# Performance work log

Hardware: AMD Instinct MI355X
Metric: run time of the kernel (lower is better)

The kernel has to match this reference:

```python
import math
import jax, jax.numpy as jnp
import numpy as np

B, S, D = 8, 920, 1536
H, HD = 4, 384            # num heads, head dim; all_head = H*HD = 1536
MAX_POS = 920
L = 2 * MAX_POS - 1       # 1839 relative positions


def setup_inputs() -> dict:
    key = jax.random.key(0)
    k1, k2, k3, k4, k5 = jax.random.split(key, 5)
    return {
        "hidden_states": jax.random.normal(k1, (B, S, D), dtype=jnp.float32),
        "w_query": jax.random.normal(k2, (D, H * HD), dtype=jnp.float32) * 0.02,
        "w_key": jax.random.normal(k3, (D, H * HD), dtype=jnp.float32) * 0.02,
        "w_value": jax.random.normal(k4, (D, H * HD), dtype=jnp.float32) * 0.02,
        "distance_embedding": jax.random.normal(k5, (L, HD), dtype=jnp.float32) * 0.02,
    }


def reshape_fortran(x, shape):
    # Matches torch reference: reverse-permute, C reshape of reversed shape, reverse-permute back.
    x = jnp.transpose(x, tuple(reversed(range(x.ndim))))
    x = jnp.reshape(x, tuple(reversed(shape)))
    return jnp.transpose(x, tuple(reversed(range(len(shape)))))


def relative_position_embedding_rotate(scores):
    # scores: [B, H, L, S]
    scores = jnp.transpose(scores, (0, 2, 3, 1))  # [B, L, S, H]
    b, hs, s, h = scores.shape
    scores = jnp.concatenate([scores, jnp.zeros((b, s, s, h), scores.dtype)], axis=1)
    scores = reshape_fortran(scores, [b, (hs + s) * s, 1, h])
    scores = scores[:, : (s + hs - 1) * s]
    scores = reshape_fortran(scores, [b, hs + s - 1, s, h])
    halfpoint = hs // 2
    scores = scores[:, halfpoint : halfpoint + s]          # [B, S, S, H]
    scores = jnp.transpose(scores, (0, 2, 1, 3))           # transpose(1,2)
    return jnp.transpose(scores, (0, 3, 1, 2))             # [B, H, S, S]


def reference(hidden_states, w_query, w_key, w_value, distance_embedding):
    inv = 1.0 / math.sqrt(HD)
    q = (hidden_states @ w_query) * inv                    # [B, S, H*HD]
    k = hidden_states @ w_key
    v = hidden_states @ w_value

    def heads(x):  # [B,S,H*HD] -> [B,H,S,HD]
        return jnp.transpose(x.reshape(B, S, H, HD), (0, 2, 1, 3))

    q, k, v = heads(q), heads(k), heads(v)

    scores = jnp.einsum("bhqd,bhkd->bhqk", q, k)           # [B,H,S,S]
    rel = jnp.einsum("ld,bhsd->bhls", distance_embedding, q)  # [B,H,L,S]
    scores = scores + relative_position_embedding_rotate(rel)

    probs = jax.nn.softmax(scores, axis=-1)
    ctx = jnp.einsum("bhqk,bhkd->bhqd", probs, v)          # [B,H,S,HD]
    ctx = jnp.transpose(ctx, (0, 2, 1, 3)).reshape(B, S, H * HD)
    return ctx
```

## Files before the change

kernel.cpp:

```cpp
#include <hip/hip_runtime.h>

#define S_LEN 920
#define DMODEL 1536
#define NH 4
#define HD 384
#define LREL 1839
#define BATCH 8
#define MTOT (BATCH * S_LEN)
#define KPAD 960
#define NBH (BATCH * NH)

#define CHS   5652480UL
#define BSLAB 2826240UL
#define KOFF  1413120UL

#define EB_BYTES 1412352UL
#define VT_BYTES 23592960UL

typedef __attribute__((ext_vector_type(8))) short  s16x8;
typedef __attribute__((ext_vector_type(4))) short  s16x4;
typedef __attribute__((ext_vector_type(8))) __bf16 bf16x8;
typedef __attribute__((ext_vector_type(4))) float  f32x4;

__device__ __forceinline__ short f2b(float x) {
  unsigned u = __builtin_bit_cast(unsigned, x);
  unsigned r = (u + 0x7FFFu + ((u >> 16) & 1u)) >> 16;
  return (short)r;
}
__device__ __forceinline__ float b2f(short s) {
  unsigned u = ((unsigned)(unsigned short)s) << 16;
  return __builtin_bit_cast(float, u);
}

__device__ __forceinline__ void load_lds16(const short* g, short* lds) {
  __builtin_amdgcn_global_load_lds(
      (const __attribute__((address_space(1))) void*)g,
      (__attribute__((address_space(3))) void*)lds, 16, 0, 0);
}

__device__ __forceinline__ f32x4 mfma_bf16(s16x8 a, s16x8 b, f32x4 c) {
  return __builtin_amdgcn_mfma_f32_16x16x32_bf16(
      __builtin_bit_cast(bf16x8, a), __builtin_bit_cast(bf16x8, b), c, 0, 0, 0);
}

__device__ __forceinline__ s16x8 frag_swz(const short* base, int row, int kk, int lq) {
  int byte = (row << 7) + (kk << 6) + (lq << 4);
  byte ^= (row & 7) << 4;
  return *(const s16x8*)((const char*)base + byte);
}

template <int NT>
__device__ __forceinline__ void gemm_pipe(short* smem,
    const short* __restrict__ A, int ldA, int mClamp, int m0,
    const short* __restrict__ B, int ldB, int nClamp, int n0,
    f32x4 acc[4][6]) {
  short* const A0 = smem;
  short* const B0 = smem + 16384;
  short* const A1 = smem + 28672;
  short* const B1 = smem + 45056;

  const int tid = threadIdx.x, w = tid >> 6, lane = tid & 63;
  const int lr = lane & 15, lq = lane >> 4;
  const int wr = w >> 1, wc = w & 1;

  const short* pa[4]; int la[4];
  const short* pb[3]; int lb[3];
  {
    const int rl = lane >> 3, c = lane & 7;
#pragma unroll
    for (int i = 0; i < 4; ++i) {
      int r = w * 32 + i * 8 + rl;
      int ra = m0 + r; if (ra > mClamp) ra = mClamp;
      pa[i] = A + (size_t)ra * ldA + ((c ^ (r & 7)) * 8);
      la[i] = (w * 32 + i * 8) * 64;
    }
#pragma unroll
    for (int i = 0; i < 3; ++i) {
      int r = w * 24 + i * 8 + rl;
      int rb = n0 + r; if (rb > nClamp) rb = nClamp;
      pb[i] = B + (size_t)rb * ldB + ((c ^ (r & 7)) * 8);
      lb[i] = (w * 24 + i * 8) * 64;
    }
  }

#pragma unroll
  for (int i = 0; i < 4; ++i)
#pragma unroll
    for (int j = 0; j < 6; ++j) acc[i][j] = (f32x4){0.f, 0.f, 0.f, 0.f};

#pragma unroll
  for (int i = 0; i < 4; ++i) load_lds16(pa[i], A0 + la[i]);
#pragma unroll
  for (int i = 0; i < 3; ++i) load_lds16(pb[i], B0 + lb[i]);

  for (int kt = 0; kt < NT; ++kt) {
    short* const Ab = (kt & 1) ? A1 : A0;
    short* const Bb = (kt & 1) ? B1 : B0;
    short* const An = (kt & 1) ? A0 : A1;
    short* const Bn = (kt & 1) ? B0 : B1;

    if (kt + 1 < NT) {
      const int k0 = (kt + 1) * 64;
#pragma unroll
      for (int i = 0; i < 4; ++i) load_lds16(pa[i] + k0, An + la[i]);
#pragma unroll
      for (int i = 0; i < 3; ++i) load_lds16(pb[i] + k0, Bn + lb[i]);
      asm volatile("s_waitcnt vmcnt(7)" ::: "memory");
    } else {
      asm volatile("s_waitcnt vmcnt(0)" ::: "memory");
    }
    __builtin_amdgcn_sched_barrier(0);
    __builtin_amdgcn_s_barrier();
    __builtin_amdgcn_sched_barrier(0);

    s16x8 a[4], bb[3];
#pragma unroll
    for (int f = 0; f < 4; ++f) a[f] = frag_swz(Ab, wr * 64 + f * 16 + lr, 0, lq);
#pragma unroll
    for (int f = 0; f < 3; ++f) bb[f] = frag_swz(Bb, wc * 96 + f * 16 + lr, 0, lq);
    __builtin_amdgcn_s_barrier();
    __builtin_amdgcn_s_setprio(1);
#pragma unroll
    for (int i = 0; i < 4; ++i)
#pragma unroll
      for (int j = 0; j < 3; ++j) acc[i][j] = mfma_bf16(a[i], bb[j], acc[i][j]);
    __builtin_amdgcn_s_setprio(0);
    __builtin_amdgcn_s_barrier();
#pragma unroll
    for (int f = 0; f < 3; ++f) bb[f] = frag_swz(Bb, wc * 96 + (3 + f) * 16 + lr, 0, lq);
    __builtin_amdgcn_s_barrier();
    __builtin_amdgcn_s_setprio(1);
#pragma unroll
    for (int i = 0; i < 4; ++i)
#pragma unroll
      for (int j = 0; j < 3; ++j) acc[i][3 + j] = mfma_bf16(a[i], bb[j], acc[i][3 + j]);
    __builtin_amdgcn_s_setprio(0);
    __builtin_amdgcn_s_barrier();
#pragma unroll
    for (int f = 0; f < 4; ++f) a[f] = frag_swz(Ab, wr * 64 + f * 16 + lr, 1, lq);
#pragma unroll
    for (int f = 0; f < 3; ++f) bb[f] = frag_swz(Bb, wc * 96 + f * 16 + lr, 1, lq);
    __builtin_amdgcn_s_barrier();
    __builtin_amdgcn_s_setprio(1);
#pragma unroll
    for (int i = 0; i < 4; ++i)
#pragma unroll
      for (int j = 0; j < 3; ++j) acc[i][j] = mfma_bf16(a[i], bb[j], acc[i][j]);
    __builtin_amdgcn_s_setprio(0);
    __builtin_amdgcn_s_barrier();
#pragma unroll
    for (int f = 0; f < 3; ++f) bb[f] = frag_swz(Bb, wc * 96 + (3 + f) * 16 + lr, 1, lq);
    __builtin_amdgcn_s_barrier();
    __builtin_amdgcn_s_setprio(1);
#pragma unroll
    for (int i = 0; i < 4; ++i)
#pragma unroll
      for (int j = 0; j < 3; ++j) acc[i][3 + j] = mfma_bf16(a[i], bb[j], acc[i][3 + j]);
    __builtin_amdgcn_s_setprio(0);
    __builtin_amdgcn_s_barrier();
  }
}

__global__ void k_cast(const float* __restrict__ X, short* __restrict__ O, int n4) {
  int i = blockIdx.x * blockDim.x + threadIdx.x;
  if (i >= n4) return;
  float4 v = ((const float4*)X)[i];
  s16x4 o = {f2b(v.x), f2b(v.y), f2b(v.z), f2b(v.w)};
  *(s16x4*)&O[(size_t)i * 4] = o;
}

__global__ void k_transpose_w(const float* __restrict__ W0, const float* __restrict__ W1,
                              const float* __restrict__ W2, short* __restrict__ Wt) {
  const float* W = (blockIdx.z == 0) ? W0 : ((blockIdx.z == 1) ? W1 : W2);
  short* O = Wt + (size_t)blockIdx.z * DMODEL * DMODEL;
  __shared__ float t[32][33];
  int tx = threadIdx.x, ty = threadIdx.y;
  int n0 = blockIdx.x * 32, k0 = blockIdx.y * 32;
#pragma unroll
  for (int i = 0; i < 4; ++i)
    t[ty + i * 8][tx] = W[(size_t)(k0 + ty + i * 8) * DMODEL + n0 + tx];
  __syncthreads();
#pragma unroll
  for (int i = 0; i < 4; ++i)
    O[(size_t)(n0 + ty + i * 8) * DMODEL + k0 + tx] = f2b(t[tx][ty + i * 8]);
}

__global__ void k_zero_vtpad(short* __restrict__ Vt) {
  int idx = blockIdx.x * blockDim.x + threadIdx.x;
  if (idx >= NBH * HD * (KPAD - S_LEN)) return;
  int bhd = idx / (KPAD - S_LEN);
  int s = S_LEN + idx - bhd * (KPAD - S_LEN);
  Vt[(size_t)bhd * KPAD + s] = 0;
}

#define QKV_NT (DMODEL / 64)

__global__ __launch_bounds__(512, 2) void k_gemm_qkv(const short* __restrict__ Xb,
                                                     const short* __restrict__ Wt,
                                                     short* __restrict__ out16,
                                                     short* __restrict__ Vt) {
  __shared__ short smem[57344];
  const int z = blockIdx.z;
  const int t = blockIdx.x;
  const int t2 = (t & 7) * 29 + (t >> 3);
  const int m0 = (t2 >> 3) * 256;
  const int n0 = (t2 & 7) * 192;

  const int tid = threadIdx.x, w = tid >> 6, lane = tid & 63;
  const int lr = lane & 15, lq = lane >> 4;
  const int wr = w >> 1, wc = w & 1;

  f32x4 acc[4][6];
  gemm_pipe<QKV_NT>(smem, Xb, DMODEL, MTOT - 1, m0,
                    Wt + (size_t)z * DMODEL * DMODEL, DMODEL, DMODEL - 1, n0, acc);

  __syncthreads();
  const float inv = 0.05103103630798287f;
  if (z != 2) {
    short* T = smem;
#pragma unroll
    for (int i = 0; i < 4; ++i)
#pragma unroll
      for (int j = 0; j < 6; ++j) {
        int ml = wr * 64 + i * 16 + lq * 4;
        int nl = wc * 96 + j * 16 + lr;
#pragma unroll
        for (int r = 0; r < 4; ++r) {
          float v = acc[i][j][r];
          T[(ml + r) * 200 + nl] = f2b(z == 0 ? v * inv : v);
        }
      }
    __syncthreads();
    for (int u = 0; u < 12; ++u) {
      int unit = u * 512 + tid;
      int ml = unit / 24, c = unit - ml * 24;
      int m = m0 + ml;
      if (m < MTOT) {
        int b = m / S_LEN, s = m - b * S_LEN;
        short* dst = out16 + (size_t)(b >> 1) * CHS + (size_t)(b & 1) * BSLAB +
                     (z == 1 ? KOFF : 0UL) + (size_t)s * DMODEL + n0 + c * 8;
        *(s16x8*)dst = *(const s16x8*)&T[ml * 200 + c * 8];
      }
    }
  } else {
    short* T = smem;
#pragma unroll
    for (int i = 0; i < 4; ++i)
#pragma unroll
      for (int j = 0; j < 6; ++j) {
        int ml = wr * 64 + i * 16 + lq * 4;
        int nl = wc * 96 + j * 16 + lr;
#pragma unroll
        for (int r = 0; r < 4; ++r)
          T[nl * 264 + ml + r] = f2b(acc[i][j][r]);
      }
    __syncthreads();
    const int h = n0 / HD;
    const int d0 = n0 - h * HD;
    for (int u = 0; u < 12; ++u) {
      int unit = u * 512 + tid;
      int nl = unit >> 5, c = unit & 31;
      int m = m0 + c * 8;
      if (m < MTOT) {
        int b = m / S_LEN, s = m - b * S_LEN;
        size_t row = (size_t)(b * NH + h) * HD + d0 + nl;
        *(s16x8*)&Vt[row * KPAD + s] = *(const s16x8*)&T[nl * 264 + c * 8];
      }
    }
  }
}

#define FKV 192
#define FNT 5

#define WAITVM(N) { asm volatile("s_waitcnt vmcnt(" #N ")" ::: "memory"); \
  __builtin_amdgcn_sched_barrier(0); __builtin_amdgcn_s_barrier(); \
  __builtin_amdgcn_sched_barrier(0); }

#define LBAR { asm volatile("s_waitcnt lgkmcnt(0)" ::: "memory"); \
  __builtin_amdgcn_sched_barrier(0); __builtin_amdgcn_s_barrier(); \
  __builtin_amdgcn_sched_barrier(0); }

#define NOISSUE { }

#define STAGE_E(BUF_, C, L0) { \
  _Pragma("unroll") for (int i_ = 0; i_ < 4; ++i_) { \
    int r_ = w * 32 + i_ * 8 + rl; \
    int rg_ = (L0) + r_; rg_ = rg_ < 0 ? 0 : (rg_ > LREL - 1 ? LREL - 1 : rg_); \
    load_lds16(Eb + (size_t)rg_ * HD + ((cs ^ (r_ & 7)) * 8) + (C) * 64, \
               (BUF_) + (w * 32 + i_ * 8) * 64); } }

#define STAGE_K(BUF_, C) { \
  _Pragma("unroll") for (int i_ = 0; i_ < 3; ++i_) { \
    int r_ = w * 24 + i_ * 8 + rl; \
    int rg_ = kv0 + r_; if (rg_ > S_LEN - 1) rg_ = S_LEN - 1; \
    load_lds16(Kp + (size_t)rg_ * DMODEL + ((cs ^ (r_ & 7)) * 8) + (C) * 64, \
               (BUF_) + (w * 24 + i_ * 8) * 64); } }

#define STAGE_V(BUF_, HF, SC) { \
  _Pragma("unroll") for (int i_ = 0; i_ < 3; ++i_) { \
    int r_ = w * 24 + i_ * 8 + rl; \
    load_lds16(Vb + (size_t)((HF) * 192 + r_) * KPAD + kv0 + (SC) * 64 + ((cs ^ (r_ & 7)) * 8), \
               (BUF_) + (w * 24 + i_ * 8) * 64); } }

#define SLOT_T(C, BUFR, ISSUE, WVM) { ISSUE; WVM; \
  s16x8 a_[2], b_[2][4]; \
  _Pragma("unroll") for (int k_ = 0; k_ < 2; ++k_) { \
    a_[k_] = frag_swz(QL + (C) * 2048, wm * 16 + lr, k_, lq); \
    _Pragma("unroll") for (int j_ = 0; j_ < 4; ++j_) \
      b_[k_][j_] = frag_swz((BUFR), wn * 64 + j_ * 16 + lr, k_, lq); } \
  __builtin_amdgcn_s_setprio(1); \
  _Pragma("unroll") for (int k_ = 0; k_ < 2; ++k_) \
    _Pragma("unroll") for (int j_ = 0; j_ < 4; ++j_) \
      acc_t[j_] = mfma_bf16(a_[k_], b_[k_][j_], acc_t[j_]); \
  __builtin_amdgcn_s_setprio(0); __builtin_amdgcn_s_barrier(); }

#define SLOT_S(C, BUFR, ISSUE, WVM) { ISSUE; WVM; \
  s16x8 a_[2], b_[2][3]; \
  _Pragma("unroll") for (int k_ = 0; k_ < 2; ++k_) { \
    a_[k_] = frag_swz(QL + (C) * 2048, wm * 16 + lr, k_, lq); \
    _Pragma("unroll") for (int j_ = 0; j_ < 3; ++j_) \
      b_[k_][j_] = frag_swz((BUFR), wn * 48 + j_ * 16 + lr, k_, lq); } \
  __builtin_amdgcn_s_setprio(1); \
  _Pragma("unroll") for (int k_ = 0; k_ < 2; ++k_) \
    _Pragma("unroll") for (int j_ = 0; j_ < 3; ++j_) \
      acc_s[j_] = mfma_bf16(a_[k_], b_[k_][j_], acc_s[j_]); \
  __builtin_amdgcn_s_setprio(0); __builtin_amdgcn_s_barrier(); }

#define SLOT_PV(SC, HF, BUFR, ISSUE, WVM) { ISSUE; WVM; \
  s16x8 a_[2], b_[2][3]; \
  _Pragma("unroll") for (int k_ = 0; k_ < 2; ++k_) { \
    a_[k_] = frag_swz(TLP + (SC) * 2048, wm * 16 + lr, k_, lq); \
    _Pragma("unroll") for (int j_ = 0; j_ < 3; ++j_) \
      b_[k_][j_] = frag_swz((BUFR), wn * 48 + j_ * 16 + lr, k_, lq); } \
  __builtin_amdgcn_s_setprio(1); \
  _Pragma("unroll") for (int k_ = 0; k_ < 2; ++k_) \
    _Pragma("unroll") for (int j_ = 0; j_ < 3; ++j_) \
      acc_o[(HF) * 3 + j_] = mfma_bf16(a_[k_], b_[k_][j_], acc_o[(HF) * 3 + j_]); \
  __builtin_amdgcn_s_setprio(0); __builtin_amdgcn_s_barrier(); }

__global__ __launch_bounds__(512, 1) void k_fused(const short* __restrict__ out16,
                                                  const short* __restrict__ Vt,
                                                  const short* __restrict__ Eb,
                                                  float* __restrict__ O, int half) {
  __shared__ short smem[70144];
  short* const QL  = smem;
  short* const B0h = smem + 12288;
  short* const B1h = smem + 28672;
  short* const B2h = smem + 45056;
  short* const TLP = smem + 61440;
  float* const pmax = (float*)(smem + 69632);
  float* const psum = pmax + 128;

  const int f  = blockIdx.x;
  const int f2 = (f & 7) * 58 + (f >> 3);
  const int mt = f2 % 29, bhl = f2 / 29;
  const int bh = half * 16 + bhl, b = bh >> 2, h = bh & 3;
  const int m0 = mt * 32;

  const int tid = threadIdx.x, w = tid >> 6, lane = tid & 63;
  const int lr = lane & 15, lq = lane >> 4;
  const int wm = w >> 2, wn = w & 3;
  const int rl = lane >> 3, cs = lane & 7;

  const short* Qp = out16 + (size_t)(b >> 1) * CHS + (size_t)(b & 1) * BSLAB + h * HD;
  const short* Kp = Qp + KOFF;
  const short* Vb = Vt + (size_t)bh * HD * KPAD;
  float* Ob = O + (size_t)bhl * S_LEN * HD;

  f32x4 acc_o[6];
  float Mst[4], Lst[4];
#pragma unroll
  for (int j = 0; j < 6; ++j) acc_o[j] = (f32x4){0.f, 0.f, 0.f, 0.f};
#pragma unroll
  for (int r = 0; r < 4; ++r) { Mst[r] = -1e30f; Lst[r] = 0.f; }

#pragma unroll
  for (int k = 0; k < 3; ++k) {
    int idx = k * 8 + w;
    int chunk = idx >> 2;
    int row = (idx & 3) * 8 + rl;
    int rg = m0 + row; if (rg > S_LEN - 1) rg = S_LEN - 1;
    load_lds16(Qp + (size_t)rg * DMODEL + chunk * 64 + ((cs ^ (row & 7)) * 8),
               QL + idx * 512);
  }
  { const int l00 = 888 - m0; STAGE_E(B0h, 0, l00); STAGE_E(B1h, 1, l00); }

  for (int t = 0; t < FNT; ++t) {
    const int kv0 = t * FKV;
    const int l0 = kv0 - m0 + 888;

    f32x4 acc_t[4];
#pragma unroll
    for (int j = 0; j < 4; ++j) acc_t[j] = (f32x4){0.f, 0.f, 0.f, 0.f};

    SLOT_T(0, B0h, STAGE_E(B2h, 2, l0), WAITVM(8));
    SLOT_T(1, B1h, STAGE_E(B0h, 3, l0), WAITVM(8));
    SLOT_T(2, B2h, STAGE_E(B1h, 4, l0), WAITVM(8));
    SLOT_T(3, B0h, STAGE_E(B2h, 5, l0), WAITVM(8));
    SLOT_T(4, B1h, STAGE_K(B0h, 0),     WAITVM(7));
    SLOT_T(5, B2h, STAGE_K(B1h, 1),     WAITVM(6));

#pragma unroll
    for (int j = 0; j < 4; ++j)
#pragma unroll
      for (int r = 0; r < 4; ++r) {
        int row = wm * 16 + lq * 4 + r;
        int col = wn * 64 + j * 16 + lr;
        TLP[row * 256 + col] = f2b(acc_t[j][r]);
      }
    LBAR;

    f32x4 acc_s[3];
#pragma unroll
    for (int j = 0; j < 3; ++j) acc_s[j] = (f32x4){0.f, 0.f, 0.f, 0.f};

    SLOT_S(0, B0h, STAGE_K(B2h, 2),    WAITVM(6));
    SLOT_S(1, B1h, STAGE_K(B0h, 3),    WAITVM(6));
    SLOT_S(2, B2h, STAGE_K(B1h, 4),    WAITVM(6));
    SLOT_S(3, B0h, STAGE_K(B2h, 5),    WAITVM(6));
    SLOT_S(4, B1h, STAGE_V(B0h, 0, 0), WAITVM(6));
    SLOT_S(5, B2h, STAGE_V(B1h, 0, 1), WAITVM(6));

#pragma unroll
    for (int j = 0; j < 3; ++j) {
      int jpl = wn * 48 + j * 16 + lr;
      int jp = kv0 + jpl;
#pragma unroll
      for (int r = 0; r < 4; ++r) {
        int row = wm * 16 + lq * 4 + r;
        float x = acc_s[j][r] + b2f(TLP[row * 256 + (jpl - row + 31)]);
        acc_s[j][r] = (jp < S_LEN) ? x : -1e30f;
      }
    }
    {
      float tm[4];
#pragma unroll
      for (int r = 0; r < 4; ++r) {
        float v = fmaxf(fmaxf(acc_s[0][r], acc_s[1][r]), acc_s[2][r]);
#pragma unroll
        for (int o = 1; o < 16; o <<= 1) v = fmaxf(v, __shfl_xor(v, o));
        tm[r] = v;
      }
      if (lr == 0) {
#pragma unroll
        for (int r = 0; r < 4; ++r)
          pmax[wn * 32 + wm * 16 + lq * 4 + r] = tm[r];
      }
    }
    LBAR;
    float fexp[4], ps[4];
#pragma unroll
    for (int r = 0; r < 4; ++r) {
      int row = wm * 16 + lq * 4 + r;
      float M2 = fmaxf(fmaxf(pmax[row], pmax[32 + row]),
                       fmaxf(pmax[64 + row], pmax[96 + row]));
      M2 = fmaxf(M2, Mst[r]);
      fexp[r] = __expf(Mst[r] - M2);
      Mst[r] = M2;
    }
#pragma unroll
    for (int r = 0; r < 4; ++r) {
      float s0 = 0.f;
#pragma unroll
      for (int j = 0; j < 3; ++j) {
        float p = __expf(acc_s[j][r] - Mst[r]);
        acc_s[j][r] = p;
        s0 += p;
      }
#pragma unroll
      for (int o = 1; o < 16; o <<= 1) s0 += __shfl_xor(s0, o);
      ps[r] = s0;
#pragma unroll
      for (int jj = 0; jj < 6; ++jj) acc_o[jj][r] *= fexp[r];
    }
    if (lr == 0) {
#pragma unroll
      for (int r = 0; r < 4; ++r)
        psum[wn * 32 + wm * 16 + lq * 4 + r] = ps[r];
    }
    LBAR;
#pragma unroll
    for (int r = 0; r < 4; ++r) {
      int row = wm * 16 + lq * 4 + r;
      float ts = psum[row] + psum[32 + row] + psum[64 + row] + psum[96 + row];
      Lst[r] = Lst[r] * fexp[r] + ts;
    }
#pragma unroll
    for (int j = 0; j < 3; ++j) {
      int c192 = wn * 48 + j * 16 + lr;
      int sc = c192 >> 6, c64 = c192 & 63;
#pragma unroll
      for (int r = 0; r < 4; ++r) {
        int row = wm * 16 + lq * 4 + r;
        int byte = sc * 4096 + row * 128 + ((c64 * 2) ^ ((row & 7) * 16));
        *(short*)((char*)TLP + byte) = f2b(acc_s[j][r]);
      }
    }
    LBAR;

    SLOT_PV(0, 0, B0h, STAGE_V(B2h, 0, 2), WAITVM(6));
    SLOT_PV(1, 0, B1h, STAGE_V(B0h, 1, 0), WAITVM(6));
    SLOT_PV(2, 0, B2h, STAGE_V(B1h, 1, 1), WAITVM(6));
    SLOT_PV(0, 1, B0h, STAGE_V(B2h, 1, 2), WAITVM(6));
    if (t < FNT - 1) {
      SLOT_PV(1, 1, B1h, STAGE_E(B0h, 0, l0 + FKV), WAITVM(7));
      SLOT_PV(2, 1, B2h, STAGE_E(B1h, 1, l0 + FKV), WAITVM(8));
    } else {
      SLOT_PV(1, 1, B1h, NOISSUE, WAITVM(3));
      SLOT_PV(2, 1, B2h, NOISSUE, WAITVM(0));
    }
  }

#pragma unroll
  for (int r = 0; r < 4; ++r) {
    int m = m0 + wm * 16 + lq * 4 + r;
    if (m < S_LEN) {
      float rs = 1.0f / Lst[r];
#pragma unroll
      for (int jj = 0; jj < 6; ++jj) {
        int d = (jj / 3) * 192 + wn * 48 + (jj % 3) * 16 + lr;
        Ob[(size_t)m * HD + d] = acc_o[jj][r] * rs;
      }
    }
  }
}

__global__ __launch_bounds__(256) void k_copy_o(const float* __restrict__ O,
                                                float* __restrict__ out, int b0) {
  int i = blockIdx.x * 256 + threadIdx.x;
  if (i >= 16 * S_LEN * HD / 4) return;
  const int per_bh = S_LEN * HD / 4;
  int bhl = i / per_bh, rem = i - bhl * per_bh;
  int m = rem / (HD / 4), d4 = rem - m * (HD / 4);
  int b = b0 + (bhl >> 2), h = bhl & 3;
  float4 v = ((const float4*)O)[i];
  ((float4*)out)[((size_t)(b * S_LEN + m) * DMODEL + h * HD + d4 * 4) >> 2] = v;
}

extern "C" void kernel_launch(void* const* d_in, const int* in_sizes, int n_in,
                              void* d_out, int out_size, void* d_ws, size_t ws_size,
                              hipStream_t stream) {
  const float* hs = (const float*)d_in[0];
  const float* wq = (const float*)d_in[1];
  const float* wk = (const float*)d_in[2];
  const float* wv = (const float*)d_in[3];
  const float* de = (const float*)d_in[4];
  char* ws = (char*)d_ws;

  short* Xb = (short*)(ws + 0);
  short* Wt = (short*)(ws + 22609920UL);
  short* Eb = (short*)(ws + 36765696UL);
  short* Vt = (short*)(ws + 36765696UL + EB_BYTES);
  float* Og = (float*)(ws + 0);
  short* out16 = (short*)d_out;

  k_cast<<<(MTOT * DMODEL / 4 + 255) / 256, 256, 0, stream>>>(hs, Xb, MTOT * DMODEL / 4);
  k_cast<<<(LREL * HD / 4 + 255) / 256, 256, 0, stream>>>(de, Eb, LREL * HD / 4);
  k_transpose_w<<<dim3(48, 48, 3), dim3(32, 8, 1), 0, stream>>>(wq, wk, wv, Wt);
  k_zero_vtpad<<<(NBH * HD * (KPAD - S_LEN) + 255) / 256, 256, 0, stream>>>(Vt);

  k_gemm_qkv<<<dim3(232, 1, 3), 512, 0, stream>>>(Xb, Wt, out16, Vt);

  for (int hf = 0; hf < 2; ++hf) {
    k_fused<<<dim3(464), 512, 0, stream>>>(out16, Vt, Eb, Og, hf);
    k_copy_o<<<dim3(5520), 256, 0, stream>>>(Og, (float*)d_out, hf * 4);
  }
}
```

Before: 435.8 us.

## Retile QKV GEMM to 192x192 with triple-buffered LDS prefetch

Replaces the 256x192 double-buffered QKV GEMM with a 192x192 tile using a three-stage LDS ring, so global loads run two k-steps ahead. The warp layout changes to 2x4 with 96x48 per warp, and the grid grows from 232 to 312 blocks per z to fill more CUs. LDS use rises to 144KB and launch bounds drop to one block per CU, which trades occupancy for deeper prefetch. The epilogue strides are adjusted to the new tile shape.

```diff
diff --git a/kernel.cpp b/kernel.cpp
--- a/kernel.cpp
+++ b/kernel.cpp
@@ -49,118 +49,6 @@
   return *(const s16x8*)((const char*)base + byte);
 }
 
-template <int NT>
-__device__ __forceinline__ void gemm_pipe(short* smem,
-    const short* __restrict__ A, int ldA, int mClamp, int m0,
-    const short* __restrict__ B, int ldB, int nClamp, int n0,
-    f32x4 acc[4][6]) {
-  short* const A0 = smem;
-  short* const B0 = smem + 16384;
-  short* const A1 = smem + 28672;
-  short* const B1 = smem + 45056;
-
-  const int tid = threadIdx.x, w = tid >> 6, lane = tid & 63;
-  const int lr = lane & 15, lq = lane >> 4;
-  const int wr = w >> 1, wc = w & 1;
-
-  const short* pa[4]; int la[4];
-  const short* pb[3]; int lb[3];
-  {
-    const int rl = lane >> 3, c = lane & 7;
-#pragma unroll
-    for (int i = 0; i < 4; ++i) {
-      int r = w * 32 + i * 8 + rl;
-      int ra = m0 + r; if (ra > mClamp) ra = mClamp;
-      pa[i] = A + (size_t)ra * ldA + ((c ^ (r & 7)) * 8);
-      la[i] = (w * 32 + i * 8) * 64;
-    }
-#pragma unroll
-    for (int i = 0; i < 3; ++i) {
-      int r = w * 24 + i * 8 + rl;
-      int rb = n0 + r; if (rb > nClamp) rb = nClamp;
-      pb[i] = B + (size_t)rb * ldB + ((c ^ (r & 7)) * 8);
-      lb[i] = (w * 24 + i * 8) * 64;
-    }
-  }
-
-#pragma unroll
-  for (int i = 0; i < 4; ++i)
-#pragma unroll
-    for (int j = 0; j < 6; ++j) acc[i][j] = (f32x4){0.f, 0.f, 0.f, 0.f};
-
-#pragma unroll
-  for (int i = 0; i < 4; ++i) load_lds16(pa[i], A0 + la[i]);
-#pragma unroll
-  for (int i = 0; i < 3; ++i) load_lds16(pb[i], B0 + lb[i]);
-
-  for (int kt = 0; kt < NT; ++kt) {
-    short* const Ab = (kt & 1) ? A1 : A0;
-    short* const Bb = (kt & 1) ? B1 : B0;
-    short* const An = (kt & 1) ? A0 : A1;
-    short* const Bn = (kt & 1) ? B0 : B1;
-
-    if (kt + 1 < NT) {
-      const int k0 = (kt + 1) * 64;
-#pragma unroll
-      for (int i = 0; i < 4; ++i) load_lds16(pa[i] + k0, An + la[i]);
-#pragma unroll
-      for (int i = 0; i < 3; ++i) load_lds16(pb[i] + k0, Bn + lb[i]);
-      asm volatile("s_waitcnt vmcnt(7)" ::: "memory");
-    } else {
-      asm volatile("s_waitcnt vmcnt(0)" ::: "memory");
-    }
-    __builtin_amdgcn_sched_barrier(0);
-    __builtin_amdgcn_s_barrier();
-    __builtin_amdgcn_sched_barrier(0);
-
-    s16x8 a[4], bb[3];
-#pragma unroll
-    for (int f = 0; f < 4; ++f) a[f] = frag_swz(Ab, wr * 64 + f * 16 + lr, 0, lq);
-#pragma unroll
-    for (int f = 0; f < 3; ++f) bb[f] = frag_swz(Bb, wc * 96 + f * 16 + lr, 0, lq);
-    __builtin_amdgcn_s_barrier();
-    __builtin_amdgcn_s_setprio(1);
-#pragma unroll
-    for (int i = 0; i < 4; ++i)
-#pragma unroll
-      for (int j = 0; j < 3; ++j) acc[i][j] = mfma_bf16(a[i], bb[j], acc[i][j]);
-    __builtin_amdgcn_s_setprio(0);
-    __builtin_amdgcn_s_barrier();
-#pragma unroll
-    for (int f = 0; f < 3; ++f) bb[f] = frag_swz(Bb, wc * 96 + (3 + f) * 16 + lr, 0, lq);
-    __builtin_amdgcn_s_barrier();
-    __builtin_amdgcn_s_setprio(1);
-#pragma unroll
-    for (int i = 0; i < 4; ++i)
-#pragma unroll
-      for (int j = 0; j < 3; ++j) acc[i][3 + j] = mfma_bf16(a[i], bb[j], acc[i][3 + j]);
-    __builtin_amdgcn_s_setprio(0);
-    __builtin_amdgcn_s_barrier();
-#pragma unroll
-    for (int f = 0; f < 4; ++f) a[f] = frag_swz(Ab, wr * 64 + f * 16 + lr, 1, lq);
-#pragma unroll
-    for (int f = 0; f < 3; ++f) bb[f] = frag_swz(Bb, wc * 96 + f * 16 + lr, 1, lq);
-    __builtin_amdgcn_s_barrier();
-    __builtin_amdgcn_s_setprio(1);
-#pragma unroll
-    for (int i = 0; i < 4; ++i)
-#pragma unroll
-      for (int j = 0; j < 3; ++j) acc[i][j] = mfma_bf16(a[i], bb[j], acc[i][j]);
-    __builtin_amdgcn_s_setprio(0);
-    __builtin_amdgcn_s_barrier();
-#pragma unroll
-    for (int f = 0; f < 3; ++f) bb[f] = frag_swz(Bb, wc * 96 + (3 + f) * 16 + lr, 1, lq);
-    __builtin_amdgcn_s_barrier();
-    __builtin_amdgcn_s_setprio(1);
-#pragma unroll
-    for (int i = 0; i < 4; ++i)
-#pragma unroll
-      for (int j = 0; j < 3; ++j) acc[i][3 + j] = mfma_bf16(a[i], bb[j], acc[i][3 + j]);
-    __builtin_amdgcn_s_setprio(0);
-    __builtin_amdgcn_s_barrier();
-  }
-}
-
 __global__ void k_cast(const float* __restrict__ X, short* __restrict__ O, int n4) {
   int i = blockIdx.x * blockDim.x + threadIdx.x;
   if (i >= n4) return;
@@ -194,36 +82,112 @@
 }
 
 #define QKV_NT (DMODEL / 64)
-
-__global__ __launch_bounds__(512, 2) void k_gemm_qkv(const short* __restrict__ Xb,
+#define QBUF   24576
+
+__global__ __launch_bounds__(512, 1) void k_gemm_qkv(const short* __restrict__ Xb,
                                                      const short* __restrict__ Wt,
                                                      short* __restrict__ out16,
                                                      short* __restrict__ Vt) {
-  __shared__ short smem[57344];
+  __shared__ short smem[73728];
   const int z = blockIdx.z;
   const int t = blockIdx.x;
-  const int t2 = (t & 7) * 29 + (t >> 3);
-  const int m0 = (t2 >> 3) * 256;
-  const int n0 = (t2 & 7) * 192;
+  const int t2 = (t & 7) * 39 + (t >> 3);
+  const int m_idx = t2 >> 3;
+  const int n_idx = t2 & 7;
+  const int m0 = m_idx * 192;
+  const int n0 = n_idx * 192;
 
   const int tid = threadIdx.x, w = tid >> 6, lane = tid & 63;
   const int lr = lane & 15, lq = lane >> 4;
-  const int wr = w >> 1, wc = w & 1;
-
-  f32x4 acc[4][6];
-  gemm_pipe<QKV_NT>(smem, Xb, DMODEL, MTOT - 1, m0,
-                    Wt + (size_t)z * DMODEL * DMODEL, DMODEL, DMODEL - 1, n0, acc);
+  const int wm = w >> 2, wn = w & 3;
+
+  const short* const Bg = Wt + (size_t)z * DMODEL * DMODEL;
+
+  const short* pa[3]; const short* pb[3]; int lofs[3];
+  {
+    const int rl = lane >> 3, c = lane & 7;
+#pragma unroll
+    for (int i = 0; i < 3; ++i) {
+      int r = w * 24 + i * 8 + rl;
+      int ra = m0 + r; if (ra > MTOT - 1) ra = MTOT - 1;
+      pa[i] = Xb + (size_t)ra * DMODEL + ((c ^ (r & 7)) * 8);
+      pb[i] = Bg + (size_t)(n0 + r) * DMODEL + ((c ^ (r & 7)) * 8);
+      lofs[i] = (w * 24 + i * 8) * 64;
+    }
+  }
+
+  f32x4 acc[6][3];
+#pragma unroll
+  for (int i = 0; i < 6; ++i)
+#pragma unroll
+    for (int j = 0; j < 3; ++j) acc[i][j] = (f32x4){0.f, 0.f, 0.f, 0.f};
+
+  short* P0 = smem;
+  short* P1 = smem + QBUF;
+  short* P2 = smem + 2 * QBUF;
+
+#pragma unroll
+  for (int i = 0; i < 3; ++i) {
+    load_lds16(pa[i], P0 + lofs[i]);
+    load_lds16(pb[i], P0 + 12288 + lofs[i]);
+  }
+#pragma unroll
+  for (int i = 0; i < 3; ++i) {
+    load_lds16(pa[i] + 64, P1 + lofs[i]);
+    load_lds16(pb[i] + 64, P1 + 12288 + lofs[i]);
+  }
+
+  for (int kt = 0; kt < QKV_NT; ++kt) {
+    short* const Ab = P0;
+    short* const Bb = P0 + 12288;
+
+    if (kt + 2 < QKV_NT) {
+      const int k0 = (kt + 2) * 64;
+#pragma unroll
+      for (int i = 0; i < 3; ++i) {
+        load_lds16(pa[i] + k0, P2 + lofs[i]);
+        load_lds16(pb[i] + k0, P2 + 12288 + lofs[i]);
+      }
+      asm volatile("s_waitcnt vmcnt(12)" ::: "memory");
+    } else if (kt + 1 < QKV_NT) {
+      asm volatile("s_waitcnt vmcnt(6)" ::: "memory");
+    } else {
+      asm volatile("s_waitcnt vmcnt(0)" ::: "memory");
+    }
+    __builtin_amdgcn_sched_barrier(0);
+    __builtin_amdgcn_s_barrier();
+    __builtin_amdgcn_sched_barrier(0);
+
+#pragma unroll
+    for (int kk = 0; kk < 2; ++kk) {
+      s16x8 a[6], bb[3];
+#pragma unroll
+      for (int f = 0; f < 6; ++f) a[f] = frag_swz(Ab, wm * 96 + f * 16 + lr, kk, lq);
+#pragma unroll
+      for (int f = 0; f < 3; ++f) bb[f] = frag_swz(Bb, wn * 48 + f * 16 + lr, kk, lq);
+      __builtin_amdgcn_s_barrier();
+      __builtin_amdgcn_s_setprio(1);
+#pragma unroll
+      for (int i = 0; i < 6; ++i)
+#pragma unroll
+        for (int j = 0; j < 3; ++j) acc[i][j] = mfma_bf16(a[i], bb[j], acc[i][j]);
+      __builtin_amdgcn_s_setprio(0);
+      __builtin_amdgcn_s_barrier();
+    }
+
+    short* tmp = P0; P0 = P1; P1 = P2; P2 = tmp;
+  }
 
   __syncthreads();
   const float inv = 0.05103103630798287f;
   if (z != 2) {
     short* T = smem;
 #pragma unroll
-    for (int i = 0; i < 4; ++i)
-#pragma unroll
-      for (int j = 0; j < 6; ++j) {
-        int ml = wr * 64 + i * 16 + lq * 4;
-        int nl = wc * 96 + j * 16 + lr;
+    for (int i = 0; i < 6; ++i)
+#pragma unroll
+      for (int j = 0; j < 3; ++j) {
+        int ml = wm * 96 + i * 16 + lq * 4;
+        int nl = wn * 48 + j * 16 + lr;
 #pragma unroll
         for (int r = 0; r < 4; ++r) {
           float v = acc[i][j][r];
@@ -231,7 +195,8 @@
         }
       }
     __syncthreads();
-    for (int u = 0; u < 12; ++u) {
+#pragma unroll
+    for (int u = 0; u < 9; ++u) {
       int unit = u * 512 + tid;
       int ml = unit / 24, c = unit - ml * 24;
       int m = m0 + ml;
@@ -245,26 +210,27 @@
   } else {
     short* T = smem;
 #pragma unroll
-    for (int i = 0; i < 4; ++i)
-#pragma unroll
-      for (int j = 0; j < 6; ++j) {
-        int ml = wr * 64 + i * 16 + lq * 4;
-        int nl = wc * 96 + j * 16 + lr;
+    for (int i = 0; i < 6; ++i)
+#pragma unroll
+      for (int j = 0; j < 3; ++j) {
+        int ml = wm * 96 + i * 16 + lq * 4;
+        int nl = wn * 48 + j * 16 + lr;
 #pragma unroll
         for (int r = 0; r < 4; ++r)
-          T[nl * 264 + ml + r] = f2b(acc[i][j][r]);
+          T[nl * 200 + ml + r] = f2b(acc[i][j][r]);
       }
     __syncthreads();
     const int h = n0 / HD;
     const int d0 = n0 - h * HD;
-    for (int u = 0; u < 12; ++u) {
+#pragma unroll
+    for (int u = 0; u < 9; ++u) {
       int unit = u * 512 + tid;
-      int nl = unit >> 5, c = unit & 31;
+      int nl = unit / 24, c = unit - nl * 24;
       int m = m0 + c * 8;
       if (m < MTOT) {
         int b = m / S_LEN, s = m - b * S_LEN;
         size_t row = (size_t)(b * NH + h) * HD + d0 + nl;
-        *(s16x8*)&Vt[row * KPAD + s] = *(const s16x8*)&T[nl * 264 + c * 8];
+        *(s16x8*)&Vt[row * KPAD + s] = *(const s16x8*)&T[nl * 200 + c * 8];
       }
     }
   }
@@ -560,7 +526,7 @@
   k_transpose_w<<<dim3(48, 48, 3), dim3(32, 8, 1), 0, stream>>>(wq, wk, wv, Wt);
   k_zero_vtpad<<<(NBH * HD * (KPAD - S_LEN) + 255) / 256, 256, 0, stream>>>(Vt);
 
-  k_gemm_qkv<<<dim3(232, 1, 3), 512, 0, stream>>>(Xb, Wt, out16, Vt);
+  k_gemm_qkv<<<dim3(312, 1, 3), 512, 0, stream>>>(Xb, Wt, out16, Vt);
 
   for (int hf = 0; hf < 2; ++hf) {
     k_fused<<<dim3(464), 512, 0, stream>>>(out16, Vt, Eb, Og, hf);
```

After: 446.4 us. +2.4%, slower.

## Load E/K/V MFMA operands directly from global memory instead of LDS staging

Applied to the files above, without the earlier changes.

Drops the triple-buffered LDS staging pipeline for the E, K and V tiles. Each wave now reads its MFMA B-fragments straight from global memory through per-lane pointers. LDS use falls from about 140KB to about 42KB, and launch bounds move from 1 to 4 blocks per CU so several blocks can share a CU. The cost is no data sharing across waves: the 2 wm-row waves each reload the same fragments. It also loses the explicit prefetch overlap, so performance now depends on cache hit rates and on occupancy hiding the global memory latency.

```diff
diff --git a/kernel.cpp b/kernel.cpp
--- a/kernel.cpp
+++ b/kernel.cpp
@@ -273,83 +273,18 @@
 #define FKV 192
 #define FNT 5
 
-#define WAITVM(N) { asm volatile("s_waitcnt vmcnt(" #N ")" ::: "memory"); \
-  __builtin_amdgcn_sched_barrier(0); __builtin_amdgcn_s_barrier(); \
-  __builtin_amdgcn_sched_barrier(0); }
-
 #define LBAR { asm volatile("s_waitcnt lgkmcnt(0)" ::: "memory"); \
   __builtin_amdgcn_sched_barrier(0); __builtin_amdgcn_s_barrier(); \
   __builtin_amdgcn_sched_barrier(0); }
 
-#define NOISSUE { }
-
-#define STAGE_E(BUF_, C, L0) { \
-  _Pragma("unroll") for (int i_ = 0; i_ < 4; ++i_) { \
-    int r_ = w * 32 + i_ * 8 + rl; \
-    int rg_ = (L0) + r_; rg_ = rg_ < 0 ? 0 : (rg_ > LREL - 1 ? LREL - 1 : rg_); \
-    load_lds16(Eb + (size_t)rg_ * HD + ((cs ^ (r_ & 7)) * 8) + (C) * 64, \
-               (BUF_) + (w * 32 + i_ * 8) * 64); } }
-
-#define STAGE_K(BUF_, C) { \
-  _Pragma("unroll") for (int i_ = 0; i_ < 3; ++i_) { \
-    int r_ = w * 24 + i_ * 8 + rl; \
-    int rg_ = kv0 + r_; if (rg_ > S_LEN - 1) rg_ = S_LEN - 1; \
-    load_lds16(Kp + (size_t)rg_ * DMODEL + ((cs ^ (r_ & 7)) * 8) + (C) * 64, \
-               (BUF_) + (w * 24 + i_ * 8) * 64); } }
-
-#define STAGE_V(BUF_, HF, SC) { \
-  _Pragma("unroll") for (int i_ = 0; i_ < 3; ++i_) { \
-    int r_ = w * 24 + i_ * 8 + rl; \
-    load_lds16(Vb + (size_t)((HF) * 192 + r_) * KPAD + kv0 + (SC) * 64 + ((cs ^ (r_ & 7)) * 8), \
-               (BUF_) + (w * 24 + i_ * 8) * 64); } }
-
-#define SLOT_T(C, BUFR, ISSUE, WVM) { ISSUE; WVM; \
-  s16x8 a_[2], b_[2][4]; \
-  _Pragma("unroll") for (int k_ = 0; k_ < 2; ++k_) { \
-    a_[k_] = frag_swz(QL + (C) * 2048, wm * 16 + lr, k_, lq); \
-    _Pragma("unroll") for (int j_ = 0; j_ < 4; ++j_) \
-      b_[k_][j_] = frag_swz((BUFR), wn * 64 + j_ * 16 + lr, k_, lq); } \
-  __builtin_amdgcn_s_setprio(1); \
-  _Pragma("unroll") for (int k_ = 0; k_ < 2; ++k_) \
-    _Pragma("unroll") for (int j_ = 0; j_ < 4; ++j_) \
-      acc_t[j_] = mfma_bf16(a_[k_], b_[k_][j_], acc_t[j_]); \
-  __builtin_amdgcn_s_setprio(0); __builtin_amdgcn_s_barrier(); }
-
-#define SLOT_S(C, BUFR, ISSUE, WVM) { ISSUE; WVM; \
-  s16x8 a_[2], b_[2][3]; \
-  _Pragma("unroll") for (int k_ = 0; k_ < 2; ++k_) { \
-    a_[k_] = frag_swz(QL + (C) * 2048, wm * 16 + lr, k_, lq); \
-    _Pragma("unroll") for (int j_ = 0; j_ < 3; ++j_) \
-      b_[k_][j_] = frag_swz((BUFR), wn * 48 + j_ * 16 + lr, k_, lq); } \
-  __builtin_amdgcn_s_setprio(1); \
-  _Pragma("unroll") for (int k_ = 0; k_ < 2; ++k_) \
-    _Pragma("unroll") for (int j_ = 0; j_ < 3; ++j_) \
-      acc_s[j_] = mfma_bf16(a_[k_], b_[k_][j_], acc_s[j_]); \
-  __builtin_amdgcn_s_setprio(0); __builtin_amdgcn_s_barrier(); }
-
-#define SLOT_PV(SC, HF, BUFR, ISSUE, WVM) { ISSUE; WVM; \
-  s16x8 a_[2], b_[2][3]; \
-  _Pragma("unroll") for (int k_ = 0; k_ < 2; ++k_) { \
-    a_[k_] = frag_swz(TLP + (SC) * 2048, wm * 16 + lr, k_, lq); \
-    _Pragma("unroll") for (int j_ = 0; j_ < 3; ++j_) \
-      b_[k_][j_] = frag_swz((BUFR), wn * 48 + j_ * 16 + lr, k_, lq); } \
-  __builtin_amdgcn_s_setprio(1); \
-  _Pragma("unroll") for (int k_ = 0; k_ < 2; ++k_) \
-    _Pragma("unroll") for (int j_ = 0; j_ < 3; ++j_) \
-      acc_o[(HF) * 3 + j_] = mfma_bf16(a_[k_], b_[k_][j_], acc_o[(HF) * 3 + j_]); \
-  __builtin_amdgcn_s_setprio(0); __builtin_amdgcn_s_barrier(); }
-
-__global__ __launch_bounds__(512, 1) void k_fused(const short* __restrict__ out16,
+__global__ __launch_bounds__(512, 4) void k_fused(const short* __restrict__ out16,
                                                   const short* __restrict__ Vt,
                                                   const short* __restrict__ Eb,
                                                   float* __restrict__ O, int half) {
-  __shared__ short smem[70144];
+  __shared__ short smem[20992];
   short* const QL  = smem;
-  short* const B0h = smem + 12288;
-  short* const B1h = smem + 28672;
-  short* const B2h = smem + 45056;
-  short* const TLP = smem + 61440;
-  float* const pmax = (float*)(smem + 69632);
+  short* const TLP = smem + 12288;
+  float* const pmax = (float*)(smem + 20480);
   float* const psum = pmax + 128;
 
   const int f  = blockIdx.x;
@@ -384,22 +319,45 @@
     load_lds16(Qp + (size_t)rg * DMODEL + chunk * 64 + ((cs ^ (row & 7)) * 8),
                QL + idx * 512);
   }
-  { const int l00 = 888 - m0; STAGE_E(B0h, 0, l00); STAGE_E(B1h, 1, l00); }
+  asm volatile("s_waitcnt vmcnt(0)" ::: "memory");
+  __builtin_amdgcn_s_barrier();
+
+  const short* vp[2][3];
+#pragma unroll
+  for (int hf = 0; hf < 2; ++hf)
+#pragma unroll
+    for (int j = 0; j < 3; ++j)
+      vp[hf][j] = Vb + (size_t)(hf * 192 + wn * 48 + j * 16 + lr) * KPAD + lq * 8;
 
   for (int t = 0; t < FNT; ++t) {
     const int kv0 = t * FKV;
     const int l0 = kv0 - m0 + 888;
 
+    const short* ep[4];
+#pragma unroll
+    for (int j = 0; j < 4; ++j) {
+      int l = l0 + wn * 64 + j * 16 + lr;
+      l = l < 0 ? 0 : (l > LREL - 1 ? LREL - 1 : l);
+      ep[j] = Eb + (size_t)l * HD + lq * 8;
+    }
     f32x4 acc_t[4];
 #pragma unroll
     for (int j = 0; j < 4; ++j) acc_t[j] = (f32x4){0.f, 0.f, 0.f, 0.f};
-
-    SLOT_T(0, B0h, STAGE_E(B2h, 2, l0), WAITVM(8));
-    SLOT_T(1, B1h, STAGE_E(B0h, 3, l0), WAITVM(8));
-    SLOT_T(2, B2h, STAGE_E(B1h, 4, l0), WAITVM(8));
-    SLOT_T(3, B0h, STAGE_E(B2h, 5, l0), WAITVM(8));
-    SLOT_T(4, B1h, STAGE_K(B0h, 0),     WAITVM(7));
-    SLOT_T(5, B2h, STAGE_K(B1h, 1),     WAITVM(6));
+#pragma unroll
+    for (int c = 0; c < 6; ++c) {
+      s16x8 bt[2][4];
+#pragma unroll
+      for (int kk = 0; kk < 2; ++kk)
+#pragma unroll
+        for (int j = 0; j < 4; ++j)
+          bt[kk][j] = *(const s16x8*)(ep[j] + c * 64 + kk * 32);
+      s16x8 a0 = frag_swz(QL + c * 2048, wm * 16 + lr, 0, lq);
+      s16x8 a1 = frag_swz(QL + c * 2048, wm * 16 + lr, 1, lq);
+#pragma unroll
+      for (int j = 0; j < 4; ++j) acc_t[j] = mfma_bf16(a0, bt[0][j], acc_t[j]);
+#pragma unroll
+      for (int j = 0; j < 4; ++j) acc_t[j] = mfma_bf16(a1, bt[1][j], acc_t[j]);
+    }
 
 #pragma unroll
     for (int j = 0; j < 4; ++j)
@@ -411,16 +369,31 @@
       }
     LBAR;
 
+    const short* kp[3];
+#pragma unroll
+    for (int j = 0; j < 3; ++j) {
+      int rg = kv0 + wn * 48 + j * 16 + lr;
+      if (rg > S_LEN - 1) rg = S_LEN - 1;
+      kp[j] = Kp + (size_t)rg * DMODEL + lq * 8;
+    }
     f32x4 acc_s[3];
 #pragma unroll
     for (int j = 0; j < 3; ++j) acc_s[j] = (f32x4){0.f, 0.f, 0.f, 0.f};
-
-    SLOT_S(0, B0h, STAGE_K(B2h, 2),    WAITVM(6));
-    SLOT_S(1, B1h, STAGE_K(B0h, 3),    WAITVM(6));
-    SLOT_S(2, B2h, STAGE_K(B1h, 4),    WAITVM(6));
-    SLOT_S(3, B0h, STAGE_K(B2h, 5),    WAITVM(6));
-    SLOT_S(4, B1h, STAGE_V(B0h, 0, 0), WAITVM(6));
-    SLOT_S(5, B2h, STAGE_V(B1h, 0, 1), WAITVM(6));
+#pragma unroll
+    for (int c = 0; c < 6; ++c) {
+      s16x8 bk[2][3];
+#pragma unroll
+      for (int kk = 0; kk < 2; ++kk)
+#pragma unroll
+        for (int j = 0; j < 3; ++j)
+          bk[kk][j] = *(const s16x8*)(kp[j] + c * 64 + kk * 32);
+      s16x8 a0 = frag_swz(QL + c * 2048, wm * 16 + lr, 0, lq);
+      s16x8 a1 = frag_swz(QL + c * 2048, wm * 16 + lr, 1, lq);
+#pragma unroll
+      for (int j = 0; j < 3; ++j) acc_s[j] = mfma_bf16(a0, bk[0][j], acc_s[j]);
+#pragma unroll
+      for (int j = 0; j < 3; ++j) acc_s[j] = mfma_bf16(a1, bk[1][j], acc_s[j]);
+    }
 
 #pragma unroll
     for (int j = 0; j < 3; ++j) {
@@ -499,17 +472,26 @@
     }
     LBAR;
 
-    SLOT_PV(0, 0, B0h, STAGE_V(B2h, 0, 2), WAITVM(6));
-    SLOT_PV(1, 0, B1h, STAGE_V(B0h, 1, 0), WAITVM(6));
-    SLOT_PV(2, 0, B2h, STAGE_V(B1h, 1, 1), WAITVM(6));
-    SLOT_PV(0, 1, B0h, STAGE_V(B2h, 1, 2), WAITVM(6));
-    if (t < FNT - 1) {
-      SLOT_PV(1, 1, B1h, STAGE_E(B0h, 0, l0 + FKV), WAITVM(7));
-      SLOT_PV(2, 1, B2h, STAGE_E(B1h, 1, l0 + FKV), WAITVM(8));
-    } else {
-      SLOT_PV(1, 1, B1h, NOISSUE, WAITVM(3));
-      SLOT_PV(2, 1, B2h, NOISSUE, WAITVM(0));
-    }
+#pragma unroll
+    for (int hf = 0; hf < 2; ++hf)
+#pragma unroll
+      for (int sc = 0; sc < 3; ++sc) {
+        s16x8 bv[2][3];
+#pragma unroll
+        for (int kk = 0; kk < 2; ++kk)
+#pragma unroll
+          for (int j = 0; j < 3; ++j)
+            bv[kk][j] = *(const s16x8*)(vp[hf][j] + kv0 + sc * 64 + kk * 32);
+        s16x8 a0 = frag_swz(TLP + sc * 2048, wm * 16 + lr, 0, lq);
+        s16x8 a1 = frag_swz(TLP + sc * 2048, wm * 16 + lr, 1, lq);
+#pragma unroll
+        for (int j = 0; j < 3; ++j)
+          acc_o[hf * 3 + j] = mfma_bf16(a0, bv[0][j], acc_o[hf * 3 + j]);
+#pragma unroll
+        for (int j = 0; j < 3; ++j)
+          acc_o[hf * 3 + j] = mfma_bf16(a1, bv[1][j], acc_o[hf * 3 + j]);
+      }
+    __syncthreads();
   }
 
 #pragma unroll
```

Measured after the change: 849.5 us. 1.95x slower.
